# Performance work log

Measured on AMD Instinct MI355X. Metric: run time of the kernel, lower is better.

The kernel has to match this reference:

```python
import jax, jax.numpy as jnp
import numpy as np

B, D, H = 64, 512, 512          # batch c, spatial dim D, feature dim H == channel
CIN = 4 * H                     # concat of 4 branches
HID = CIN // 4                  # reduction=4


def _gcn_norm_adj():
    # fixed 4-node fully-connected graph, GCNConv default: add self loops,
    # symmetric normalization D^{-1/2} (A+I) D^{-1/2}
    ei = np.array([[0, 1, 0, 2, 0, 3, 1, 2, 1, 3, 2, 3],
                   [1, 0, 2, 0, 3, 0, 2, 1, 3, 1, 3, 2]])
    A = np.zeros((4, 4), np.float32)
    A[ei[1], ei[0]] = 1.0               # message src -> dst
    A += np.eye(4, dtype=np.float32)    # self loops
    dinv = 1.0 / np.sqrt(A.sum(1))
    return jnp.asarray(dinv[:, None] * A * dinv[None, :])  # (4,4)


def setup_inputs() -> dict:
    key = jax.random.key(0)
    ks = jax.random.split(key, 32)

    def rn(k, shape, s=0.02):
        return jax.random.normal(k, shape, dtype=jnp.float32) * s

    inp = {}
    for i in range(4):
        inp[f"fea{i+1}"] = jax.random.normal(ks[i], (B, D, H), dtype=jnp.float32)
    inp["W_gcn"] = rn(ks[4], (H, H))
    inp["b_gcn"] = jnp.zeros((H,), jnp.float32)
    for i in range(4):
        inp[f"W1_{i+1}"] = rn(ks[5 + 4 * i], (CIN, HID))
        inp[f"b1_{i+1}"] = jnp.zeros((HID,), jnp.float32)
        inp[f"W2_{i+1}"] = rn(ks[6 + 4 * i], (HID, H))
        inp[f"b2_{i+1}"] = jnp.zeros((H,), jnp.float32)
    return inp


def reference(fea1, fea2, fea3, fea4, W_gcn, b_gcn,
              W1_1, b1_1, W2_1, b2_1,
              W1_2, b1_2, W2_2, b2_2,
              W1_3, b1_3, W2_3, b2_3,
              W1_4, b1_4, W2_4, b2_4):
    A = _gcn_norm_adj()                                   # (4,4)
    y = jnp.stack((fea1, fea2, fea3, fea4), axis=1)       # (B,4,D,H)
    # GCNConv batched over all samples: Ahat_norm @ (X W) + b
    xw = jnp.einsum('bndh,hk->bndk', y, W_gcn)            # (B,4,D,H)
    yg = jnp.einsum('mn,bndk->bmdk', A, xw) + b_gcn       # (B,4,D,H)
    z = jnp.concatenate([yg[:, 0], yg[:, 1], yg[:, 2], yg[:, 3]], axis=2)  # (B,D,4H)

    def gate(W1, b1, W2, b2, fea):
        h = jax.nn.relu(z @ W1 + b1)                      # (B,D,HID)
        g = jax.nn.sigmoid(h @ W2 + b2)                   # (B,D,H)
        return jax.nn.relu(g) * fea

    return (gate(W1_1, b1_1, W2_1, b2_1, fea1),
            gate(W1_2, b1_2, W2_2, b2_2, fea2),
            gate(W1_3, b1_3, W2_3, b2_3, fea3),
            gate(W1_4, b1_4, W2_4, b2_4, fea4))
```

## Files before the change

kernel.cpp:

```cpp
#include <hip/hip_runtime.h>
#include <math.h>

#define MM 32768
#define KK 512
#define NN 512
#define BM 128
#define BN 128
#define BK 32

typedef float  f32x4  __attribute__((ext_vector_type(4)));
typedef __bf16 bf16x8 __attribute__((ext_vector_type(8)));
typedef unsigned short u16x8 __attribute__((ext_vector_type(8)));

__device__ __forceinline__ unsigned short f2bf(float f) {
    union { float f; unsigned int u; } v; v.f = f;
    unsigned int r = v.u + 0x7fffu + ((v.u >> 16) & 1u);
    return (unsigned short)(r >> 16);
}

__device__ __forceinline__ void gl_lds16(const void* g, void* l) {
    __builtin_amdgcn_global_load_lds((const __attribute__((address_space(1))) void*)g,
                                     (__attribute__((address_space(3))) void*)l,
                                     16, 0, 0);
}

__global__ __launch_bounds__(256)
void fsum_cast(const float* __restrict__ f1, const float* __restrict__ f2,
               const float* __restrict__ f3, const float* __restrict__ f4,
               unsigned short* __restrict__ out)
{
    const long i = ((long)blockIdx.x * 256 + threadIdx.x) * 8;
    f32x4 s0 = *(const f32x4*)(f1 + i);
    f32x4 s1 = *(const f32x4*)(f1 + i + 4);
    s0 += *(const f32x4*)(f2 + i);  s1 += *(const f32x4*)(f2 + i + 4);
    s0 += *(const f32x4*)(f3 + i);  s1 += *(const f32x4*)(f3 + i + 4);
    s0 += *(const f32x4*)(f4 + i);  s1 += *(const f32x4*)(f4 + i + 4);
    u16x8 o;
    o[0] = f2bf(s0[0]); o[1] = f2bf(s0[1]); o[2] = f2bf(s0[2]); o[3] = f2bf(s0[3]);
    o[4] = f2bf(s1[0]); o[5] = f2bf(s1[1]); o[6] = f2bf(s1[2]); o[7] = f2bf(s1[3]);
    *(u16x8*)(out + i) = o;
}

struct WArgs {
    const float* src[9];
    unsigned short* dst[9];
};

__global__ __launch_bounds__(256)
void wprep(WArgs a)
{
    __shared__ float t[32][33];
    const int z  = blockIdx.z;
    const float* __restrict__ src = a.src[z];
    unsigned short* __restrict__ dst = a.dst[z];
    const int k0 = blockIdx.x * 32;
    const int n0 = blockIdx.y * 32;
    const int tx = threadIdx.x;
    for (int kk = threadIdx.y; kk < 32; kk += 8) {
        float v = src[(long)(k0 + kk) * 512 + n0 + tx];
        if (z >= 1 && z <= 4) {
            v += src[(long)(512  + k0 + kk) * 512 + n0 + tx];
            v += src[(long)(1024 + k0 + kk) * 512 + n0 + tx];
            v += src[(long)(1536 + k0 + kk) * 512 + n0 + tx];
        }
        if (z == 0) v *= 0.25f;
        t[kk][tx] = v;
    }
    __syncthreads();
    for (int nn = threadIdx.y; nn < 32; nn += 8) {
        dst[(long)(n0 + nn) * 512 + k0 + tx] = f2bf(t[tx][nn]);
    }
}

template<int MODE>
__global__ __launch_bounds__(256)
void gemm_ep(const unsigned short* __restrict__ A,
             const unsigned short* __restrict__ Bt,
             const float* __restrict__ bias,
             const float* __restrict__ fea,
             void* __restrict__ out)
{
    __shared__ unsigned short As[BM * BK];
    __shared__ unsigned short Bs[BN * BK];

    const int tid  = threadIdx.x;
    const int lane = tid & 63;
    const int wave = tid >> 6;
    const int m0 = blockIdx.x * BM;
    const int n0 = blockIdx.y * BN;

    const bool isA = (wave < 2);
    const int rowbase = (wave & 1) * 64;
    const unsigned short* gsrc = isA ? A : Bt;
    unsigned short* ldst = isA ? As : Bs;
    const int r  = lane >> 2;
    const int cb = lane & 3;
    const long grow0 = (isA ? (long)m0 : (long)n0) + rowbase;
    const unsigned short* gbase0 = gsrc + grow0 * KK + cb * 8;
    unsigned short* lbase = ldst + rowbase * BK;

    const int frow = lane & 15;
    const int fk   = (lane >> 4) * 8;
    const int wrow = wave >> 1;
    const int wcol = wave & 1;

    f32x4 acc[4][4] = {};

    for (int ks = 0; ks < KK / BK; ++ks) {
        const unsigned short* gb = gbase0 + ks * BK;
        #pragma unroll
        for (int c = 0; c < 4; ++c) {
            gl_lds16(gb + (long)(c * 16 + r) * KK, lbase + c * 16 * BK);
        }
        __syncthreads();

        bf16x8 afr[4], bfr[4];
        #pragma unroll
        for (int i = 0; i < 4; ++i)
            afr[i] = *(const bf16x8*)(As + (wrow * 64 + i * 16 + frow) * BK + fk);
        #pragma unroll
        for (int j = 0; j < 4; ++j)
            bfr[j] = *(const bf16x8*)(Bs + (wcol * 64 + j * 16 + frow) * BK + fk);

        #pragma unroll
        for (int i = 0; i < 4; ++i)
            #pragma unroll
            for (int j = 0; j < 4; ++j)
                acc[i][j] = __builtin_amdgcn_mfma_f32_16x16x32_bf16(
                    afr[i], bfr[j], acc[i][j], 0, 0, 0);
        __syncthreads();
    }

    const int cq = (lane >> 4) * 4;
    const int cc = lane & 15;
    #pragma unroll
    for (int j = 0; j < 4; ++j) {
        const int col = n0 + wcol * 64 + j * 16 + cc;
        const float bv = bias[col];
        #pragma unroll
        for (int i = 0; i < 4; ++i) {
            #pragma unroll
            for (int rr = 0; rr < 4; ++rr) {
                const int row = m0 + wrow * 64 + i * 16 + cq + rr;
                float v = acc[i][j][rr] + bv;
                if (MODE == 0) {
                    ((unsigned short*)out)[(long)row * NN + col] = f2bf(v);
                } else if (MODE == 1) {
                    ((unsigned short*)out)[(long)row * NN + col] = f2bf(fmaxf(v, 0.0f));
                } else {
                    const float g = 1.0f / (1.0f + __expf(-v));
                    ((float*)out)[(long)row * NN + col] =
                        g * fea[(long)row * NN + col];
                }
            }
        }
    }
}

extern "C" void kernel_launch(void* const* d_in, const int* in_sizes, int n_in,
                              void* d_out, int out_size, void* d_ws, size_t ws_size,
                              hipStream_t stream)
{
    (void)in_sizes; (void)n_in; (void)out_size; (void)ws_size;

    const float* fea[4] = {(const float*)d_in[0], (const float*)d_in[1],
                           (const float*)d_in[2], (const float*)d_in[3]};
    const float* W_gcn = (const float*)d_in[4];
    const float* b_gcn = (const float*)d_in[5];
    const float *W1[4], *b1[4], *W2[4], *b2[4];
    for (int i = 0; i < 4; ++i) {
        W1[i] = (const float*)d_in[6 + 4 * i];
        b1[i] = (const float*)d_in[7 + 4 * i];
        W2[i] = (const float*)d_in[8 + 4 * i];
        b2[i] = (const float*)d_in[9 + 4 * i];
    }

    char* ws = (char*)d_ws;
    unsigned short* fsum_h = (unsigned short*)ws;
    unsigned short* s_buf  = (unsigned short*)(ws + (size_t)33554432);
    unsigned short* wbuf   = (unsigned short*)(ws + (size_t)67108864);
    unsigned short* WgT = wbuf;
    unsigned short *W1T[4], *W2T[4];
    for (int i = 0; i < 4; ++i) {
        W1T[i] = wbuf + (size_t)(1 + i) * 262144;
        W2T[i] = wbuf + (size_t)(5 + i) * 262144;
    }

    fsum_cast<<<8192, 256, 0, stream>>>(fea[0], fea[1], fea[2], fea[3], fsum_h);

    WArgs wa;
    wa.src[0] = W_gcn; wa.dst[0] = WgT;
    for (int i = 0; i < 4; ++i) { wa.src[1 + i] = W1[i]; wa.dst[1 + i] = W1T[i]; }
    for (int i = 0; i < 4; ++i) { wa.src[5 + i] = W2[i]; wa.dst[5 + i] = W2T[i]; }
    wprep<<<dim3(16, 16, 9), dim3(32, 8), 0, stream>>>(wa);

    const dim3 ggrid(MM / BM, NN / BN);
    gemm_ep<0><<<ggrid, 256, 0, stream>>>(fsum_h, WgT, b_gcn, nullptr, s_buf);

    float* outp = (float*)d_out;
    for (int i = 0; i < 4; ++i) {
        gemm_ep<1><<<ggrid, 256, 0, stream>>>(s_buf, W1T[i], b1[i], nullptr, fsum_h);
        gemm_ep<2><<<ggrid, 256, 0, stream>>>(fsum_h, W2T[i], b2[i], fea[i],
                                              outp + (size_t)i * MM * NN);
    }
}
```

Measured before the change: 857.7 us.

## Batch four gate branches into single launches and double GEMM K-tile depth

The four per-branch W1 and W2 GEMM launches become one launch each. The W1 stage treats the stacked W1 weights as a single N=2048 GEMM writing into a separate h buffer, and the W2 stage uses a z-grid dimension to select the branch. The K tile doubles from 32 to 64, which halves the barrier and load rounds per tile, and each tile now runs two MFMA sub-steps. This cuts launch count and tail effects and exposes more concurrent blocks, in exchange for more LDS per block (32KB) and a larger workspace footprint.

Result: slower. 967.0 us (+12.7%).

```diff
diff --git a/kernel.cpp b/kernel.cpp
--- a/kernel.cpp
+++ b/kernel.cpp
@@ -3,10 +3,9 @@
 
 #define MM 32768
 #define KK 512
-#define NN 512
 #define BM 128
 #define BN 128
-#define BK 32
+#define BK 64
 
 typedef float  f32x4  __attribute__((ext_vector_type(4)));
 typedef __bf16 bf16x8 __attribute__((ext_vector_type(8)));
@@ -72,13 +71,17 @@
     }
 }
 
+struct GArgs {
+    const unsigned short* Az[4];
+    const unsigned short* Bt;
+    const float* bias[4];
+    const float* fea[4];
+    void* out;
+};
+
 template<int MODE>
 __global__ __launch_bounds__(256)
-void gemm_ep(const unsigned short* __restrict__ A,
-             const unsigned short* __restrict__ Bt,
-             const float* __restrict__ bias,
-             const float* __restrict__ fea,
-             void* __restrict__ out)
+void gemm_ep(GArgs a)
 {
     __shared__ unsigned short As[BM * BK];
     __shared__ unsigned short Bs[BN * BK];
@@ -88,15 +91,19 @@
     const int wave = tid >> 6;
     const int m0 = blockIdx.x * BM;
     const int n0 = blockIdx.y * BN;
+    const int zz = (MODE == 2) ? blockIdx.z : ((MODE == 1) ? (n0 >> 9) : 0);
+
+    const unsigned short* A  = a.Az[(MODE == 2) ? zz : 0];
+    const unsigned short* Bt = (MODE == 2) ? (a.Bt + (size_t)zz * 512 * 512) : a.Bt;
 
     const bool isA = (wave < 2);
     const int rowbase = (wave & 1) * 64;
     const unsigned short* gsrc = isA ? A : Bt;
     unsigned short* ldst = isA ? As : Bs;
-    const int r  = lane >> 2;
-    const int cb = lane & 3;
+    const int r8 = lane >> 3;
+    const int s8 = lane & 7;
     const long grow0 = (isA ? (long)m0 : (long)n0) + rowbase;
-    const unsigned short* gbase0 = gsrc + grow0 * KK + cb * 8;
+    const unsigned short* gbase0 = gsrc + (grow0 + r8) * KK + s8 * 8;
     unsigned short* lbase = ldst + rowbase * BK;
 
     const int frow = lane & 15;
@@ -109,34 +116,40 @@
     for (int ks = 0; ks < KK / BK; ++ks) {
         const unsigned short* gb = gbase0 + ks * BK;
         #pragma unroll
-        for (int c = 0; c < 4; ++c) {
-            gl_lds16(gb + (long)(c * 16 + r) * KK, lbase + c * 16 * BK);
+        for (int c = 0; c < 8; ++c) {
+            gl_lds16(gb + (long)(c * 8) * KK, lbase + c * 8 * BK);
         }
         __syncthreads();
 
-        bf16x8 afr[4], bfr[4];
         #pragma unroll
-        for (int i = 0; i < 4; ++i)
-            afr[i] = *(const bf16x8*)(As + (wrow * 64 + i * 16 + frow) * BK + fk);
-        #pragma unroll
-        for (int j = 0; j < 4; ++j)
-            bfr[j] = *(const bf16x8*)(Bs + (wcol * 64 + j * 16 + frow) * BK + fk);
-
-        #pragma unroll
-        for (int i = 0; i < 4; ++i)
+        for (int hh = 0; hh < 2; ++hh) {
+            bf16x8 afr[4], bfr[4];
+            #pragma unroll
+            for (int i = 0; i < 4; ++i)
+                afr[i] = *(const bf16x8*)(As + (wrow * 64 + i * 16 + frow) * BK
+                                             + hh * 32 + fk);
             #pragma unroll
             for (int j = 0; j < 4; ++j)
-                acc[i][j] = __builtin_amdgcn_mfma_f32_16x16x32_bf16(
-                    afr[i], bfr[j], acc[i][j], 0, 0, 0);
+                bfr[j] = *(const bf16x8*)(Bs + (wcol * 64 + j * 16 + frow) * BK
+                                             + hh * 32 + fk);
+            #pragma unroll
+            for (int i = 0; i < 4; ++i)
+                #pragma unroll
+                for (int j = 0; j < 4; ++j)
+                    acc[i][j] = __builtin_amdgcn_mfma_f32_16x16x32_bf16(
+                        afr[i], bfr[j], acc[i][j], 0, 0, 0);
+        }
         __syncthreads();
     }
 
     const int cq = (lane >> 4) * 4;
     const int cc = lane & 15;
+    const float* bias_p = a.bias[zz];
     #pragma unroll
     for (int j = 0; j < 4; ++j) {
         const int col = n0 + wcol * 64 + j * 16 + cc;
-        const float bv = bias[col];
+        const int coll = col & 511;
+        const float bv = bias_p[coll];
         #pragma unroll
         for (int i = 0; i < 4; ++i) {
             #pragma unroll
@@ -144,13 +157,14 @@
                 const int row = m0 + wrow * 64 + i * 16 + cq + rr;
                 float v = acc[i][j][rr] + bv;
                 if (MODE == 0) {
-                    ((unsigned short*)out)[(long)row * NN + col] = f2bf(v);
+                    ((unsigned short*)a.out)[(long)row * 512 + col] = f2bf(v);
                 } else if (MODE == 1) {
-                    ((unsigned short*)out)[(long)row * NN + col] = f2bf(fmaxf(v, 0.0f));
+                    ((unsigned short*)a.out)[((long)zz * MM + row) * 512 + coll]
+                        = f2bf(fmaxf(v, 0.0f));
                 } else {
                     const float g = 1.0f / (1.0f + __expf(-v));
-                    ((float*)out)[(long)row * NN + col] =
-                        g * fea[(long)row * NN + col];
+                    ((float*)a.out)[((long)zz * MM + row) * 512 + col]
+                        = g * a.fea[zz][(long)row * 512 + col];
                 }
             }
         }
@@ -176,31 +190,40 @@
     }
 
     char* ws = (char*)d_ws;
-    unsigned short* fsum_h = (unsigned short*)ws;
+    unsigned short* fsum_b = (unsigned short*)ws;
     unsigned short* s_buf  = (unsigned short*)(ws + (size_t)33554432);
-    unsigned short* wbuf   = (unsigned short*)(ws + (size_t)67108864);
-    unsigned short* WgT = wbuf;
-    unsigned short *W1T[4], *W2T[4];
-    for (int i = 0; i < 4; ++i) {
-        W1T[i] = wbuf + (size_t)(1 + i) * 262144;
-        W2T[i] = wbuf + (size_t)(5 + i) * 262144;
-    }
-
-    fsum_cast<<<8192, 256, 0, stream>>>(fea[0], fea[1], fea[2], fea[3], fsum_h);
+    unsigned short* h_buf  = (unsigned short*)(ws + (size_t)67108864);
+    unsigned short* wbuf   = (unsigned short*)(ws + (size_t)201326592);
+    unsigned short* WgT     = wbuf;
+    unsigned short* W1T_all = wbuf + (size_t)262144;
+    unsigned short* W2T_all = wbuf + (size_t)5 * 262144;
+
+    fsum_cast<<<8192, 256, 0, stream>>>(fea[0], fea[1], fea[2], fea[3], fsum_b);
 
     WArgs wa;
     wa.src[0] = W_gcn; wa.dst[0] = WgT;
-    for (int i = 0; i < 4; ++i) { wa.src[1 + i] = W1[i]; wa.dst[1 + i] = W1T[i]; }
-    for (int i = 0; i < 4; ++i) { wa.src[5 + i] = W2[i]; wa.dst[5 + i] = W2T[i]; }
+    for (int i = 0; i < 4; ++i) {
+        wa.src[1 + i] = W1[i]; wa.dst[1 + i] = W1T_all + (size_t)i * 262144;
+        wa.src[5 + i] = W2[i]; wa.dst[5 + i] = W2T_all + (size_t)i * 262144;
+    }
     wprep<<<dim3(16, 16, 9), dim3(32, 8), 0, stream>>>(wa);
 
-    const dim3 ggrid(MM / BM, NN / BN);
-    gemm_ep<0><<<ggrid, 256, 0, stream>>>(fsum_h, WgT, b_gcn, nullptr, s_buf);
-
-    float* outp = (float*)d_out;
+    GArgs g0 = {};
+    g0.Az[0] = fsum_b; g0.Bt = WgT; g0.bias[0] = b_gcn; g0.out = s_buf;
+    gemm_ep<0><<<dim3(MM / BM, 4), 256, 0, stream>>>(g0);
+
+    GArgs g1 = {};
+    g1.Az[0] = s_buf; g1.Bt = W1T_all;
+    for (int i = 0; i < 4; ++i) g1.bias[i] = b1[i];
+    g1.out = h_buf;
+    gemm_ep<1><<<dim3(MM / BM, 16), 256, 0, stream>>>(g1);
+
+    GArgs g2 = {};
     for (int i = 0; i < 4; ++i) {
-        gemm_ep<1><<<ggrid, 256, 0, stream>>>(s_buf, W1T[i], b1[i], nullptr, fsum_h);
-        gemm_ep<2><<<ggrid, 256, 0, stream>>>(fsum_h, W2T[i], b2[i], fea[i],
-                                              outp + (size_t)i * MM * NN);
-    }
-}
+        g2.Az[i]   = h_buf + (size_t)i * MM * 512;
+        g2.bias[i] = b2[i];
+        g2.fea[i]  = fea[i];
+    }
+    g2.Bt = W2T_all; g2.out = d_out;
+    gemm_ep<2><<<dim3(MM / BM, 4, 4), 256, 0, stream>>>(g2);
+}
```
